# Kernel tuning notes

Hardware: AMD Instinct MI355X
Metric: run time of the kernel (lower is better)

## Reference

```python
import jax, jax.numpy as jnp
import numpy as np

NUM_USERS = 100000
NUM_ITEMS = 50000
NUM_EDGES = 4000000
EMB_DIM = 64
K_HOPS = 3


def setup_inputs() -> dict:
    key = jax.random.key(0)
    k1, k2, k3, k4, k5, k6 = jax.random.split(key, 6)
    N = NUM_USERS + NUM_ITEMS
    return {
        "users_emb": jax.random.normal(k1, (NUM_USERS, EMB_DIM), dtype=jnp.float32) * 0.1,
        "items_emb": jax.random.normal(k2, (NUM_ITEMS, EMB_DIM), dtype=jnp.float32) * 0.1,
        "edge_row": jax.random.randint(k3, (NUM_EDGES,), 0, N, dtype=jnp.int32),
        "edge_col": jax.random.randint(k4, (NUM_EDGES,), 0, N, dtype=jnp.int32),
        "user_id": jax.random.randint(k5, (4096,), 0, NUM_USERS, dtype=jnp.int32),
        "item_ids": jax.random.randint(k6, (4096,), 0, NUM_ITEMS, dtype=jnp.int32),
    }


def reference(users_emb, items_emb, edge_row, edge_col, user_id, item_ids):
    num_users = users_emb.shape[0]
    N = num_users + items_emb.shape[0]
    dt = users_emb.dtype

    # gcn_norm (no self loops): deg = rowsum of A, w_e = d_r^{-1/2} d_c^{-1/2}
    deg = jax.ops.segment_sum(jnp.ones(edge_row.shape[0], dtype=dt), edge_row,
                              num_segments=N)
    deg_inv_sqrt = jnp.where(deg > 0, 1.0 / jnp.sqrt(jnp.where(deg > 0, deg, 1.0)), 0.0)
    w = deg_inv_sqrt[edge_row] * deg_inv_sqrt[edge_col]  # [E]

    emb = jnp.concatenate([users_emb, items_emb], axis=0)  # [N, D]
    acc = emb  # running sum of K+1 layer snapshots
    for _ in range(K_HOPS):
        # SpMM: out[r] += w_e * emb[c]
        emb = jax.ops.segment_sum(w[:, None] * emb[edge_col], edge_row,
                                  num_segments=N)
        acc = acc + emb
    emb_final = acc / (K_HOPS + 1)  # layer-mean pooling

    users_final = emb_final[user_id]               # [B, D]
    items_final = emb_final[num_users + item_ids]  # [B, D]
    return jnp.concatenate([users_final, items_final], axis=1)  # [B, 2D]
```

## Files before the change

kernel.cpp:

```cpp
#include <hip/hip_runtime.h>
#include <hip/hip_bf16.h>

#define NUSERS 100000
#define NITEMS 50000
#define NN (NUSERS + NITEMS)
#define NE 4000000
#define DIM 64
#define BQ 4096
#define NBIN ((NN + 255) >> 8)
#define BINCAP 9216
#define EPB2 12288

typedef unsigned short u16;
typedef unsigned int u32;
typedef float v2f __attribute__((ext_vector_type(2)));
typedef unsigned u32x2 __attribute__((ext_vector_type(2)));

#if __has_builtin(__builtin_nontemporal_load)
#define NTLOAD(p) __builtin_nontemporal_load(p)
#else
#define NTLOAD(p) (*(p))
#endif

__device__ __forceinline__ float bf2f(u16 u) {
    return __uint_as_float(((unsigned)u) << 16);
}
__device__ __forceinline__ u16 f2bf(float f) {
    unsigned x = __float_as_uint(f);
    return (u16)((x + 0x7FFFu + ((x >> 16) & 1u)) >> 16);
}
__device__ __forceinline__ void add8p(v2f* acc2, uint4 u) {
    acc2[0] += (v2f){__uint_as_float(u.x << 16), __uint_as_float(u.x & 0xffff0000u)};
    acc2[1] += (v2f){__uint_as_float(u.y << 16), __uint_as_float(u.y & 0xffff0000u)};
    acc2[2] += (v2f){__uint_as_float(u.z << 16), __uint_as_float(u.z & 0xffff0000u)};
    acc2[3] += (v2f){__uint_as_float(u.w << 16), __uint_as_float(u.w & 0xffff0000u)};
}

#if __has_builtin(__builtin_amdgcn_update_dpp)
__device__ __forceinline__ float xadd8(float x) {
    int y = __builtin_amdgcn_update_dpp(0, __float_as_int(x), 0x128, 0xF, 0xF, true);
    return x + __int_as_float(y);
}
#else
__device__ __forceinline__ float xadd8(float x) { return x + __shfl_xor(x, 8, 64); }
#endif
#if __has_builtin(__builtin_amdgcn_permlane16_swap)
__device__ __forceinline__ float xadd16(float x) {
    u32x2 r = __builtin_amdgcn_permlane16_swap(__float_as_uint(x), __float_as_uint(x),
                                               false, false);
    return __uint_as_float(r.x) + __uint_as_float(r.y);
}
#else
__device__ __forceinline__ float xadd16(float x) { return x + __shfl_xor(x, 16, 64); }
#endif

#if __has_builtin(__builtin_amdgcn_sched_barrier)
#define SCHED_FENCE() __builtin_amdgcn_sched_barrier(0)
#else
#define SCHED_FENCE()
#endif

__device__ __forceinline__ void reduce_half(v2f* acc2) {
#pragma unroll
    for (int j = 0; j < 4; ++j) { acc2[j].x = xadd8(acc2[j].x);  acc2[j].y = xadd8(acc2[j].y);  }
#pragma unroll
    for (int j = 0; j < 4; ++j) { acc2[j].x = xadd16(acc2[j].x); acc2[j].y = xadd16(acc2[j].y); }
}

__device__ __forceinline__ void batch8(const int* __restrict__ col_s, int start,
                                       int s0, int lim, int eslot,
                                       const char* __restrict__ base2, v2f* acc2) {
    int cg[8];
#pragma unroll
    for (int g = 0; g < 8; ++g) {
        int slot = s0 + (g << 2) + eslot;
        int c = NTLOAD(col_s + start + slot);
        cg[g] = (slot < lim) ? c : NN;
    }
    uint4 v[8];
#pragma unroll
    for (int g = 0; g < 8; ++g)
        v[g] = *(const uint4*)(base2 + (((u32)cg[g]) << 7));
    SCHED_FENCE();
#pragma unroll
    for (int g = 0; g < 8; ++g) add8p(acc2, v[g]);
}

template<bool MASKED>
__global__ void __launch_bounds__(256) k_spmm2(
        const int2* __restrict__ meta2, const int* __restrict__ col_s,
        const u16* __restrict__ in, u16* __restrict__ out,
        const unsigned char* __restrict__ mask) {
    int wid = (blockIdx.x * blockDim.x + threadIdx.x) >> 6;
    int lane = threadIdx.x & 63;
    int half = lane >> 5;
    int eslot = (lane >> 3) & 3;
    int dg = lane & 7;
    int r = (wid << 1) + half;
    int2 mv = meta2[r];
    int start = mv.x, n = mv.y;
    int m = MASKED ? (int)mask[r] : 1;
    int n8 = (n + 7) & ~7;
    int lim = m ? n8 : 0;
    if (MASKED && !__any(lim > 0)) return;
    const char* base2 = (const char*)in + (dg << 4);

    v2f acc2[4] = {(v2f)0.f, (v2f)0.f, (v2f)0.f, (v2f)0.f};
    batch8(col_s, start, 0, lim, eslot, base2, acc2);
    if (__any(lim > 32))
        batch8(col_s, start, 32, lim, eslot, base2, acc2);
    if (__any(lim > 64)) {
        for (int i = 64 + eslot; i < lim; i += 4) {
            int c = col_s[start + i];
            uint4 u = *(const uint4*)(base2 + (((u32)c) << 7));
            add8p(acc2, u);
        }
    }
    reduce_half(acc2);
    if (eslot == 0 && m) {
        float sc = (n > 0) ? (1.0f / (float)n) : 0.0f;
        v2f vs = {sc, sc};
        u32 p[4];
#pragma unroll
        for (int j = 0; j < 4; ++j) {
            v2f t = acc2[j] * vs;
            __hip_bfloat162 h = __float22bfloat162_rn(make_float2(t.x, t.y));
            p[j] = *(u32*)&h;
        }
        ((uint4*)out)[(size_t)r * 8 + dg] = make_uint4(p[0], p[1], p[2], p[3]);
    }
}

__global__ void __launch_bounds__(256) k_spmm_out2(
        const int2* __restrict__ meta2, const int* __restrict__ col_s,
        const u16* __restrict__ in, const int* __restrict__ uid,
        const int* __restrict__ iid, float* __restrict__ out) {
    int wid = (blockIdx.x * blockDim.x + threadIdx.x) >> 6;
    int lane = threadIdx.x & 63;
    int half = lane >> 5;
    int eslot = (lane >> 3) & 3;
    int dg = lane & 7;
    int q = (wid << 1) + half;
    int b, r, off;
    if (q < BQ) { b = q; r = uid[q]; off = 0; }
    else { b = q - BQ; r = NUSERS + iid[q - BQ]; off = DIM; }
    int2 mv = meta2[r];
    int start = mv.x, n = mv.y;
    int n8 = (n + 7) & ~7;
    const char* base2 = (const char*)in + (dg << 4);

    v2f acc2[4] = {(v2f)0.f, (v2f)0.f, (v2f)0.f, (v2f)0.f};
    batch8(col_s, start, 0, n8, eslot, base2, acc2);
    if (__any(n8 > 32))
        batch8(col_s, start, 32, n8, eslot, base2, acc2);
    if (__any(n8 > 64)) {
        for (int i = 64 + eslot; i < n8; i += 4) {
            int c = col_s[start + i];
            uint4 u = *(const uint4*)(base2 + (((u32)c) << 7));
            add8p(acc2, u);
        }
    }
    reduce_half(acc2);
    if (eslot == 0) {
        float dr = (n > 0) ? (1.0f / sqrtf((float)n)) : 0.0f;
        float* o = out + (size_t)b * (2 * DIM) + off + dg * 8;
#pragma unroll
        for (int j = 0; j < 4; ++j) {
            o[2 * j]     = (o[2 * j]     + dr * acc2[j].x) * 0.25f;
            o[2 * j + 1] = (o[2 * j + 1] + dr * acc2[j].y) * 0.25f;
        }
    }
}

__global__ void k_init(int* __restrict__ bin_cur, u32* __restrict__ m2w,
                       u16* __restrict__ ea, u16* __restrict__ eb) {
    int t = blockIdx.x * blockDim.x + threadIdx.x;
    if (t < NBIN) bin_cur[t] = t * BINCAP;
    if (t < 37504) m2w[t] = 0;
    if (t < 32) {
        ((u32*)(ea + (size_t)NN * DIM))[t] = 0;
        ((u32*)(eb + (size_t)NN * DIM))[t] = 0;
    }
}

__global__ void __launch_bounds__(1024) k_binA2(
        const int* __restrict__ row, const int* __restrict__ col,
        int* __restrict__ bin_cur, u32* __restrict__ pairs, int E) {
    __shared__ u32 stage[EPB2];
    __shared__ int hist[NBIN];
    __shared__ int base_l[NBIN];
    __shared__ int cbase[NBIN];
    __shared__ int lcur[NBIN];
    __shared__ int s[1024];
    int t = threadIdx.x;
    int base = blockIdx.x * EPB2;
    int lim = min(E - base, EPB2);
    int n4 = lim >> 2;

    if (t < NBIN) hist[t] = 0;
    __syncthreads();

    for (int i = t; i < n4; i += 1024) {
        int4 r4 = ((const int4*)(row + base))[i];
        atomicAdd(&hist[r4.x >> 8], 1);
        atomicAdd(&hist[r4.y >> 8], 1);
        atomicAdd(&hist[r4.z >> 8], 1);
        atomicAdd(&hist[r4.w >> 8], 1);
    }
    for (int i = (n4 << 2) + t; i < lim; i += 1024)
        atomicAdd(&hist[row[base + i] >> 8], 1);
    __syncthreads();

    int v = (t < NBIN) ? hist[t] : 0;
    s[t] = v;
    __syncthreads();
    for (int off = 1; off < 1024; off <<= 1) {
        int x = (t >= off) ? s[t - off] : 0;
        __syncthreads();
        s[t] += x;
        __syncthreads();
    }
    if (t < NBIN) {
        int excl = s[t] - v;
        base_l[t] = excl;
        lcur[t] = excl;
        cbase[t] = (v > 0) ? atomicAdd(&bin_cur[t], v) : 0;
    }
    __syncthreads();

    for (int i = t; i < n4; i += 1024) {
        int4 r4 = ((const int4*)(row + base))[i];
        int4 c4 = ((const int4*)(col + base))[i];
        int pos;
        pos = atomicAdd(&lcur[r4.x >> 8], 1);
        stage[pos] = ((u32)(r4.x & 255) << 24) | (u32)c4.x;
        pos = atomicAdd(&lcur[r4.y >> 8], 1);
        stage[pos] = ((u32)(r4.y & 255) << 24) | (u32)c4.y;
        pos = atomicAdd(&lcur[r4.z >> 8], 1);
        stage[pos] = ((u32)(r4.z & 255) << 24) | (u32)c4.z;
        pos = atomicAdd(&lcur[r4.w >> 8], 1);
        stage[pos] = ((u32)(r4.w & 255) << 24) | (u32)c4.w;
    }
    for (int i = (n4 << 2) + t; i < lim; i += 1024) {
        int r = row[base + i];
        int c = col[base + i];
        int pos = atomicAdd(&lcur[r >> 8], 1);
        stage[pos] = ((u32)(r & 255) << 24) | (u32)c;
    }
    __syncthreads();

    int wv = t >> 6;
    int lane = t & 63;
    for (int b = wv; b < NBIN; b += 16) {
        int h = hist[b];
        int lb = base_l[b];
        size_t gb = (size_t)cbase[b];
        for (int i = lane; i < h; i += 64)
            pairs[gb + i] = stage[lb + i];
    }
}

__global__ void __launch_bounds__(1024) k_binB(
        const u32* __restrict__ pairs, const int* __restrict__ bin_cur,
        int* __restrict__ col_s, int* __restrict__ rs, int* __restrict__ deg,
        int2* __restrict__ meta2) {
    __shared__ int cnt[256];
    __shared__ int pscan[256];
    __shared__ int cur[256];
    int b = blockIdx.x;
    int t = threadIdx.x;
    int base = b * BINCAP;
    int end = bin_cur[b];
    int cnt4 = (end - base) >> 2;
    if (t < 256) cnt[t] = 0;
    __syncthreads();
    for (int i = t; i < cnt4; i += 1024) {
        uint4 p4 = ((const uint4*)(pairs + base))[i];
        atomicAdd(&cnt[p4.x >> 24], 1);
        atomicAdd(&cnt[p4.y >> 24], 1);
        atomicAdd(&cnt[p4.z >> 24], 1);
        atomicAdd(&cnt[p4.w >> 24], 1);
    }
    for (int i = base + (cnt4 << 2) + t; i < end; i += 1024)
        atomicAdd(&cnt[pairs[i] >> 24], 1);
    __syncthreads();
    int v = (t < 256) ? cnt[t] : 0;
    int pv = (v + 7) & ~7;
    if (t < 256) pscan[t] = pv;
    __syncthreads();
    for (int off = 1; off < 256; off <<= 1) {
        int x = (t >= off && t < 256) ? pscan[t - off] : 0;
        __syncthreads();
        if (t < 256) pscan[t] += x;
        __syncthreads();
    }
    if (t < 256) {
        int rowstart = base + pscan[t] - pv;
        int r = (b << 8) + t;
        if (r < NN) {
            rs[r] = rowstart;
            deg[r] = v;
            meta2[r] = make_int2(rowstart, v);
        }
        cur[t] = rowstart;
        for (int i = v; i < pv; ++i) col_s[rowstart + i] = NN;
    }
    __syncthreads();
    for (int i = t; i < cnt4; i += 1024) {
        uint4 p4 = ((const uint4*)(pairs + base))[i];
        int pos;
        pos = atomicAdd(&cur[p4.x >> 24], 1);
        col_s[pos] = (int)(p4.x & 0x00FFFFFFu);
        pos = atomicAdd(&cur[p4.y >> 24], 1);
        col_s[pos] = (int)(p4.y & 0x00FFFFFFu);
        pos = atomicAdd(&cur[p4.z >> 24], 1);
        col_s[pos] = (int)(p4.z & 0x00FFFFFFu);
        pos = atomicAdd(&cur[p4.w >> 24], 1);
        col_s[pos] = (int)(p4.w & 0x00FFFFFFu);
    }
    for (int i = base + (cnt4 << 2) + t; i < end; i += 1024) {
        u32 p = pairs[i];
        int pos = atomicAdd(&cur[p >> 24], 1);
        col_s[pos] = (int)(p & 0x00FFFFFFu);
    }
}

__global__ void k_concat_t0(const float* __restrict__ u, const float* __restrict__ it,
                            const int* __restrict__ deg, u16* __restrict__ emb) {
    int i = blockIdx.x * blockDim.x + threadIdx.x;
    const int NU4 = NUSERS * DIM / 4;
    const int NT4 = NN * DIM / 4;
    if (i >= NT4) return;
    int row = i >> 4;
    int d = deg[row];
    float sc = (d > 0) ? (1.0f / sqrtf((float)d)) : 0.0f;
    float4 v = (i < NU4) ? ((const float4*)u)[i] : ((const float4*)it)[i - NU4];
    ushort4 o;
    o.x = f2bf(sc * v.x); o.y = f2bf(sc * v.y);
    o.z = f2bf(sc * v.z); o.w = f2bf(sc * v.w);
    ((ushort4*)emb)[i] = o;
}

__global__ void k_mark(const int* __restrict__ uid, const int* __restrict__ iid,
                       const int* __restrict__ rs, const int* __restrict__ deg,
                       const int* __restrict__ col_s, unsigned char* __restrict__ m2) {
    int q = (blockIdx.x * blockDim.x + threadIdx.x) >> 6;
    if (q >= 2 * BQ) return;
    int lane = threadIdx.x & 63;
    int r = (q < BQ) ? uid[q] : (NUSERS + iid[q - BQ]);
    if (lane == 0) m2[r] = 1;
    int s = rs[r], n = deg[r];
    for (int i = lane; i < n; i += 64) m2[col_s[s + i]] = 1;
}


__global__ void k_gather_init(const int* __restrict__ uid, const int* __restrict__ iid,
                              const float* __restrict__ u, const float* __restrict__ it,
                              float* __restrict__ out) {
    int t = blockIdx.x * blockDim.x + threadIdx.x;
    if (t >= BQ * DIM) return;
    int b = t >> 6;
    int d = t & 63;
    out[b * (2 * DIM) + d]       = u[(size_t)uid[b] * DIM + d];
    out[b * (2 * DIM) + DIM + d] = it[(size_t)iid[b] * DIM + d];
}

__global__ void k_gather_add(const int* __restrict__ uid, const int* __restrict__ iid,
                             const int* __restrict__ deg, const u16* __restrict__ emb,
                             float* __restrict__ out) {
    int t = blockIdx.x * blockDim.x + threadIdx.x;
    if (t >= BQ * DIM) return;
    int b = t >> 6;
    int d = t & 63;
    int ru = uid[b];
    int ri = NUSERS + iid[b];
    int du = deg[ru], di = deg[ri];
    float su = (du > 0) ? sqrtf((float)du) : 0.0f;
    float si = (di > 0) ? sqrtf((float)di) : 0.0f;
    int ou = b * (2 * DIM) + d;
    int oi = ou + DIM;
    out[ou] = out[ou] + su * bf2f(emb[(size_t)ru * DIM + d]);
    out[oi] = out[oi] + si * bf2f(emb[(size_t)ri * DIM + d]);
}


extern "C" void kernel_launch(void* const* d_in, const int* in_sizes, int n_in,
                              void* d_out, int out_size, void* d_ws, size_t ws_size,
                              hipStream_t stream) {
    const float* users_emb = (const float*)d_in[0];
    const float* items_emb = (const float*)d_in[1];
    const int*   edge_row  = (const int*)d_in[2];
    const int*   edge_col  = (const int*)d_in[3];
    const int*   user_id   = (const int*)d_in[4];
    const int*   item_ids  = (const int*)d_in[5];
    float* out = (float*)d_out;

    char* ws = (char*)d_ws;
    int*   deg_i   = (int*)  (ws + 0);
    int*   rs      = (int*)  (ws + 655360);
    int*   bin_cur = (int*)  (ws + 1310720);
    unsigned char* m2 = (unsigned char*)(ws + 1400000);
    int2*  meta2   = (int2*) (ws + 2097152);
    int*   col_s   = (int*)  (ws + 4194304);
    u32*   pairs   = (u32*)  (ws + 29360128);
    u16*   emb_a   = (u16*)  (ws + 54525952);
    u16*   emb_b   = (u16*)  (ws + 75497472);

    k_init<<<147, 256, 0, stream>>>(bin_cur, (u32*)m2, emb_a, emb_b);

    k_binA2<<<(NE + EPB2 - 1) / EPB2, 1024, 0, stream>>>(edge_row, edge_col, bin_cur,
                                                         pairs, NE);
    k_binB<<<NBIN, 1024, 0, stream>>>(pairs, bin_cur, col_s, rs, deg_i, meta2);

    k_concat_t0<<<(NN * DIM / 4 + 255) / 256, 256, 0, stream>>>(users_emb, items_emb,
                                                                deg_i, emb_a);

    k_gather_init<<<(BQ * DIM + 255) / 256, 256, 0, stream>>>(user_id, item_ids,
                                                              users_emb, items_emb, out);

    k_mark<<<(2 * BQ + 3) / 4, 256, 0, stream>>>(user_id, item_ids, rs, deg_i, col_s, m2);

    k_spmm2<false><<<18750, 256, 0, stream>>>(meta2, col_s, emb_a, emb_b,
                                              (const unsigned char*)nullptr);
    k_gather_add<<<(BQ * DIM + 255) / 256, 256, 0, stream>>>(user_id, item_ids, deg_i,
                                                             emb_b, out);
    k_spmm2<true><<<18750, 256, 0, stream>>>(meta2, col_s, emb_b, emb_a, m2);
    k_gather_add<<<(BQ * DIM + 255) / 256, 256, 0, stream>>>(user_id, item_ids, deg_i,
                                                             emb_a, out);
    k_spmm_out2<<<1024, 256, 0, stream>>>(meta2, col_s, emb_a, user_id, item_ids, out);
}
```

Baseline: 298.6 us.

## Sort CSR columns by sub-bin, persistent SpMM loop, fuse gather init

Within each row, binB now counts and places edges by column slice (col>>13), so a row's neighbor list is roughly sorted by column. This aims to improve cache locality of the embedding gathers, at the cost of 19x larger shared histograms and more atomics. The SpMM becomes a grid-stride persistent kernel with 2048 blocks and a simple 8-wide loop in place of the batch8 unrolled gathers, trading memory-level parallelism for lower launch cost and higher occupancy. Nontemporal loads are dropped, and the gather_init kernel is folded into the first gather_add.

```diff
diff --git a/kernel.cpp b/kernel.cpp
--- a/kernel.cpp
+++ b/kernel.cpp
@@ -10,17 +10,15 @@
 #define NBIN ((NN + 255) >> 8)
 #define BINCAP 9216
 #define EPB2 12288
+#define NSL 19
+#define SPMM_BLOCKS 2048
+#define ROWS_PER_ITER (SPMM_BLOCKS * 8)
+#define SPMM_ITERS ((NN + ROWS_PER_ITER - 1) / ROWS_PER_ITER)
 
 typedef unsigned short u16;
 typedef unsigned int u32;
 typedef float v2f __attribute__((ext_vector_type(2)));
 typedef unsigned u32x2 __attribute__((ext_vector_type(2)));
-
-#if __has_builtin(__builtin_nontemporal_load)
-#define NTLOAD(p) __builtin_nontemporal_load(p)
-#else
-#define NTLOAD(p) (*(p))
-#endif
 
 __device__ __forceinline__ float bf2f(u16 u) {
     return __uint_as_float(((unsigned)u) << 16);
@@ -67,6 +65,58 @@
     for (int j = 0; j < 4; ++j) { acc2[j].x = xadd16(acc2[j].x); acc2[j].y = xadd16(acc2[j].y); }
 }
 
+template<bool MASKED>
+__global__ void __launch_bounds__(256, 8) k_spmm2(
+        const int2* __restrict__ meta2, const int* __restrict__ col_s,
+        const u16* __restrict__ in, u16* __restrict__ out,
+        const unsigned char* __restrict__ mask) {
+    int lane = threadIdx.x & 63;
+    int half = lane >> 5;
+    int eslot = (lane >> 3) & 3;
+    int dg = lane & 7;
+    const char* base2 = (const char*)in + (dg << 4);
+    int rb0 = (blockIdx.x << 3) + ((threadIdx.x >> 7) << 2) + (((threadIdx.x >> 6) & 1) << 1) + half;
+#pragma unroll 1
+    for (int it = 0; it < SPMM_ITERS; ++it) {
+        int r = rb0 + it * ROWS_PER_ITER;
+        if (r >= NN) break;
+        int2 mv = meta2[r];
+        int start = mv.x, n = mv.y;
+        int m = MASKED ? (int)mask[r] : 1;
+        int n8 = (n + 7) & ~7;
+        int lim = m ? n8 : 0;
+        if (!__any(lim > 0)) continue;
+
+        v2f acc2[4] = {(v2f)0.f, (v2f)0.f, (v2f)0.f, (v2f)0.f};
+#pragma unroll 1
+        for (int i = 0; __any(i < lim); i += 8) {
+            int s0 = i + eslot;
+            int s1 = i + 4 + eslot;
+            int c0 = col_s[start + s0];
+            int c1 = col_s[start + s1];
+            c0 = (s0 < lim) ? c0 : NN;
+            c1 = (s1 < lim) ? c1 : NN;
+            uint4 v0 = *(const uint4*)(base2 + (((u32)c0) << 7));
+            uint4 v1 = *(const uint4*)(base2 + (((u32)c1) << 7));
+            add8p(acc2, v0);
+            add8p(acc2, v1);
+        }
+        reduce_half(acc2);
+        if (eslot == 0 && m) {
+            float sc = (n > 0) ? (1.0f / (float)n) : 0.0f;
+            v2f vs = {sc, sc};
+            u32 p[4];
+#pragma unroll
+            for (int j = 0; j < 4; ++j) {
+                v2f t = acc2[j] * vs;
+                __hip_bfloat162 h = __float22bfloat162_rn(make_float2(t.x, t.y));
+                p[j] = *(u32*)&h;
+            }
+            ((uint4*)out)[(size_t)r * 8 + dg] = make_uint4(p[0], p[1], p[2], p[3]);
+        }
+    }
+}
+
 __device__ __forceinline__ void batch8(const int* __restrict__ col_s, int start,
                                        int s0, int lim, int eslot,
                                        const char* __restrict__ base2, v2f* acc2) {
@@ -74,7 +124,7 @@
 #pragma unroll
     for (int g = 0; g < 8; ++g) {
         int slot = s0 + (g << 2) + eslot;
-        int c = NTLOAD(col_s + start + slot);
+        int c = col_s[start + slot];
         cg[g] = (slot < lim) ? c : NN;
     }
     uint4 v[8];
@@ -84,51 +134,6 @@
     SCHED_FENCE();
 #pragma unroll
     for (int g = 0; g < 8; ++g) add8p(acc2, v[g]);
-}
-
-template<bool MASKED>
-__global__ void __launch_bounds__(256) k_spmm2(
-        const int2* __restrict__ meta2, const int* __restrict__ col_s,
-        const u16* __restrict__ in, u16* __restrict__ out,
-        const unsigned char* __restrict__ mask) {
-    int wid = (blockIdx.x * blockDim.x + threadIdx.x) >> 6;
-    int lane = threadIdx.x & 63;
-    int half = lane >> 5;
-    int eslot = (lane >> 3) & 3;
-    int dg = lane & 7;
-    int r = (wid << 1) + half;
-    int2 mv = meta2[r];
-    int start = mv.x, n = mv.y;
-    int m = MASKED ? (int)mask[r] : 1;
-    int n8 = (n + 7) & ~7;
-    int lim = m ? n8 : 0;
-    if (MASKED && !__any(lim > 0)) return;
-    const char* base2 = (const char*)in + (dg << 4);
-
-    v2f acc2[4] = {(v2f)0.f, (v2f)0.f, (v2f)0.f, (v2f)0.f};
-    batch8(col_s, start, 0, lim, eslot, base2, acc2);
-    if (__any(lim > 32))
-        batch8(col_s, start, 32, lim, eslot, base2, acc2);
-    if (__any(lim > 64)) {
-        for (int i = 64 + eslot; i < lim; i += 4) {
-            int c = col_s[start + i];
-            uint4 u = *(const uint4*)(base2 + (((u32)c) << 7));
-            add8p(acc2, u);
-        }
-    }
-    reduce_half(acc2);
-    if (eslot == 0 && m) {
-        float sc = (n > 0) ? (1.0f / (float)n) : 0.0f;
-        v2f vs = {sc, sc};
-        u32 p[4];
-#pragma unroll
-        for (int j = 0; j < 4; ++j) {
-            v2f t = acc2[j] * vs;
-            __hip_bfloat162 h = __float22bfloat162_rn(make_float2(t.x, t.y));
-            p[j] = *(u32*)&h;
-        }
-        ((uint4*)out)[(size_t)r * 8 + dg] = make_uint4(p[0], p[1], p[2], p[3]);
-    }
 }
 
 __global__ void __launch_bounds__(256) k_spmm_out2(
@@ -264,28 +269,34 @@
         const u32* __restrict__ pairs, const int* __restrict__ bin_cur,
         int* __restrict__ col_s, int* __restrict__ rs, int* __restrict__ deg,
         int2* __restrict__ meta2) {
-    __shared__ int cnt[256];
+    __shared__ int cnt2[256 * NSL];
+    __shared__ int cur2[256 * NSL];
     __shared__ int pscan[256];
-    __shared__ int cur[256];
     int b = blockIdx.x;
     int t = threadIdx.x;
     int base = b * BINCAP;
     int end = bin_cur[b];
     int cnt4 = (end - base) >> 2;
-    if (t < 256) cnt[t] = 0;
+    for (int i = t; i < 256 * NSL; i += 1024) cnt2[i] = 0;
     __syncthreads();
     for (int i = t; i < cnt4; i += 1024) {
         uint4 p4 = ((const uint4*)(pairs + base))[i];
-        atomicAdd(&cnt[p4.x >> 24], 1);
-        atomicAdd(&cnt[p4.y >> 24], 1);
-        atomicAdd(&cnt[p4.z >> 24], 1);
-        atomicAdd(&cnt[p4.w >> 24], 1);
-    }
-    for (int i = base + (cnt4 << 2) + t; i < end; i += 1024)
-        atomicAdd(&cnt[pairs[i] >> 24], 1);
-    __syncthreads();
-    int v = (t < 256) ? cnt[t] : 0;
-    int pv = (v + 7) & ~7;
+        atomicAdd(&cnt2[(p4.x >> 24) * NSL + ((p4.x & 0xFFFFFFu) >> 13)], 1);
+        atomicAdd(&cnt2[(p4.y >> 24) * NSL + ((p4.y & 0xFFFFFFu) >> 13)], 1);
+        atomicAdd(&cnt2[(p4.z >> 24) * NSL + ((p4.z & 0xFFFFFFu) >> 13)], 1);
+        atomicAdd(&cnt2[(p4.w >> 24) * NSL + ((p4.w & 0xFFFFFFu) >> 13)], 1);
+    }
+    for (int i = base + (cnt4 << 2) + t; i < end; i += 1024) {
+        u32 p = pairs[i];
+        atomicAdd(&cnt2[(p >> 24) * NSL + ((p & 0xFFFFFFu) >> 13)], 1);
+    }
+    __syncthreads();
+    int tot = 0;
+    if (t < 256) {
+#pragma unroll
+        for (int sl = 0; sl < NSL; ++sl) tot += cnt2[t * NSL + sl];
+    }
+    int pv = (tot + 7) & ~7;
     if (t < 256) pscan[t] = pv;
     __syncthreads();
     for (int off = 1; off < 256; off <<= 1) {
@@ -299,28 +310,33 @@
         int r = (b << 8) + t;
         if (r < NN) {
             rs[r] = rowstart;
-            deg[r] = v;
-            meta2[r] = make_int2(rowstart, v);
-        }
-        cur[t] = rowstart;
-        for (int i = v; i < pv; ++i) col_s[rowstart + i] = NN;
+            deg[r] = tot;
+            meta2[r] = make_int2(rowstart, tot);
+        }
+        int run = rowstart;
+#pragma unroll
+        for (int sl = 0; sl < NSL; ++sl) {
+            cur2[t * NSL + sl] = run;
+            run += cnt2[t * NSL + sl];
+        }
+        for (int i = tot; i < pv; ++i) col_s[rowstart + i] = NN;
     }
     __syncthreads();
     for (int i = t; i < cnt4; i += 1024) {
         uint4 p4 = ((const uint4*)(pairs + base))[i];
         int pos;
-        pos = atomicAdd(&cur[p4.x >> 24], 1);
+        pos = atomicAdd(&cur2[(p4.x >> 24) * NSL + ((p4.x & 0xFFFFFFu) >> 13)], 1);
         col_s[pos] = (int)(p4.x & 0x00FFFFFFu);
-        pos = atomicAdd(&cur[p4.y >> 24], 1);
+        pos = atomicAdd(&cur2[(p4.y >> 24) * NSL + ((p4.y & 0xFFFFFFu) >> 13)], 1);
         col_s[pos] = (int)(p4.y & 0x00FFFFFFu);
-        pos = atomicAdd(&cur[p4.z >> 24], 1);
+        pos = atomicAdd(&cur2[(p4.z >> 24) * NSL + ((p4.z & 0xFFFFFFu) >> 13)], 1);
         col_s[pos] = (int)(p4.z & 0x00FFFFFFu);
-        pos = atomicAdd(&cur[p4.w >> 24], 1);
+        pos = atomicAdd(&cur2[(p4.w >> 24) * NSL + ((p4.w & 0xFFFFFFu) >> 13)], 1);
         col_s[pos] = (int)(p4.w & 0x00FFFFFFu);
     }
     for (int i = base + (cnt4 << 2) + t; i < end; i += 1024) {
         u32 p = pairs[i];
-        int pos = atomicAdd(&cur[p >> 24], 1);
+        int pos = atomicAdd(&cur2[(p >> 24) * NSL + ((p & 0xFFFFFFu) >> 13)], 1);
         col_s[pos] = (int)(p & 0x00FFFFFFu);
     }
 }
@@ -353,20 +369,10 @@
     for (int i = lane; i < n; i += 64) m2[col_s[s + i]] = 1;
 }
 
-
-__global__ void k_gather_init(const int* __restrict__ uid, const int* __restrict__ iid,
-                              const float* __restrict__ u, const float* __restrict__ it,
-                              float* __restrict__ out) {
-    int t = blockIdx.x * blockDim.x + threadIdx.x;
-    if (t >= BQ * DIM) return;
-    int b = t >> 6;
-    int d = t & 63;
-    out[b * (2 * DIM) + d]       = u[(size_t)uid[b] * DIM + d];
-    out[b * (2 * DIM) + DIM + d] = it[(size_t)iid[b] * DIM + d];
-}
-
+template<bool INIT>
 __global__ void k_gather_add(const int* __restrict__ uid, const int* __restrict__ iid,
                              const int* __restrict__ deg, const u16* __restrict__ emb,
+                             const float* __restrict__ u, const float* __restrict__ it,
                              float* __restrict__ out) {
     int t = blockIdx.x * blockDim.x + threadIdx.x;
     if (t >= BQ * DIM) return;
@@ -379,8 +385,10 @@
     float si = (di > 0) ? sqrtf((float)di) : 0.0f;
     int ou = b * (2 * DIM) + d;
     int oi = ou + DIM;
-    out[ou] = out[ou] + su * bf2f(emb[(size_t)ru * DIM + d]);
-    out[oi] = out[oi] + si * bf2f(emb[(size_t)ri * DIM + d]);
+    float bu = INIT ? u[(size_t)ru * DIM + d] : out[ou];
+    float bi = INIT ? it[(size_t)(ri - NUSERS) * DIM + d] : out[oi];
+    out[ou] = bu + su * bf2f(emb[(size_t)ru * DIM + d]);
+    out[oi] = bi + si * bf2f(emb[(size_t)ri * DIM + d]);
 }
 
 
@@ -415,17 +423,14 @@
     k_concat_t0<<<(NN * DIM / 4 + 255) / 256, 256, 0, stream>>>(users_emb, items_emb,
                                                                 deg_i, emb_a);
 
-    k_gather_init<<<(BQ * DIM + 255) / 256, 256, 0, stream>>>(user_id, item_ids,
-                                                              users_emb, items_emb, out);
-
     k_mark<<<(2 * BQ + 3) / 4, 256, 0, stream>>>(user_id, item_ids, rs, deg_i, col_s, m2);
 
-    k_spmm2<false><<<18750, 256, 0, stream>>>(meta2, col_s, emb_a, emb_b,
-                                              (const unsigned char*)nullptr);
-    k_gather_add<<<(BQ * DIM + 255) / 256, 256, 0, stream>>>(user_id, item_ids, deg_i,
-                                                             emb_b, out);
-    k_spmm2<true><<<18750, 256, 0, stream>>>(meta2, col_s, emb_b, emb_a, m2);
-    k_gather_add<<<(BQ * DIM + 255) / 256, 256, 0, stream>>>(user_id, item_ids, deg_i,
-                                                             emb_a, out);
+    k_spmm2<false><<<SPMM_BLOCKS, 256, 0, stream>>>(meta2, col_s, emb_a, emb_b,
+                                                    (const unsigned char*)nullptr);
+    k_gather_add<true><<<(BQ * DIM + 255) / 256, 256, 0, stream>>>(
+        user_id, item_ids, deg_i, emb_b, users_emb, items_emb, out);
+    k_spmm2<true><<<SPMM_BLOCKS, 256, 0, stream>>>(meta2, col_s, emb_b, emb_a, m2);
+    k_gather_add<false><<<(BQ * DIM + 255) / 256, 256, 0, stream>>>(
+        user_id, item_ids, deg_i, emb_a, users_emb, items_emb, out);
     k_spmm_out2<<<1024, 256, 0, stream>>>(meta2, col_s, emb_a, user_id, item_ids, out);
 }
```

Result: slower. 307.4 us (+2.9%).
